# Kernel tuning notes

Hardware: AMD Instinct MI355X
Metric: run time of the kernel (lower is better)

## Reference

```python
import jax, jax.numpy as jnp
import numpy as np

B, Q, KV = 4, 256, 1024
QS, KS, H, VS = 128, 128, 128, 256

def setup_inputs() -> dict:
    key = jax.random.key(0)
    ks = jax.random.split(key, 7)
    return {
        "queries": jax.random.normal(ks[0], (B, Q, QS), dtype=jnp.float32),
        "keys": jax.random.normal(ks[1], (B, KV, KS), dtype=jnp.float32),
        "values": jax.random.normal(ks[2], (B, KV, VS), dtype=jnp.float32),
        "valid_lens": jax.random.randint(ks[3], (B,), 0, KV, dtype=jnp.int64 if jax.config.read('jax_enable_x64') else jnp.int32),
        "Wq": jax.random.normal(ks[4], (QS, H), dtype=jnp.float32),
        "Wk": jax.random.normal(ks[5], (KS, H), dtype=jnp.float32),
        "wv": jax.random.normal(ks[6], (H,), dtype=jnp.float32),
    }

def reference(queries, keys, values, valid_lens, Wq, Wk, wv):
    # project: [B,Q,H], [B,KV,H]
    q = jnp.einsum('bqd,dh->bqh', queries, Wq)
    k = jnp.einsum('bkd,dh->bkh', keys, Wk)
    # additive scores: broadcast add -> tanh -> reduce with w_v  [B,Q,KV]
    feats = jnp.tanh(q[:, :, None, :] + k[:, None, :, :])  # [B,Q,KV,H]
    scores = jnp.einsum('bqkh,h->bqk', feats, wv)
    # masked softmax over KV with value -1e6 at masked slots
    mask = jnp.arange(scores.shape[-1])[None, None, :] < valid_lens[:, None, None]
    scores = jnp.where(mask, scores, -1e6)
    attn = jax.nn.softmax(scores, axis=-1)
    # weighted sum of values  [B,Q,VS]
    return jnp.einsum('bqk,bkv->bqv', attn, values)
```

## Files before the change

kernel.cpp:

```cpp
#include <hip/hip_runtime.h>

#define LOG2E   1.4426950408889634f

__global__ __launch_bounds__(256) void proj_kernel(
    const float* __restrict__ q_in, const float* __restrict__ k_in,
    const float* __restrict__ Wq, const float* __restrict__ Wk,
    const int* __restrict__ valid_lens,
    float* __restrict__ qc, float* __restrict__ kct)
{
    __shared__ __align__(16) float x_s[8][128];
    __shared__ __align__(16) float ps[4][8][128];
    int tid = threadIdx.x;
    int blk = blockIdx.x;
    bool is_q = (blk < 128);
    int r0 = (is_q ? blk : blk - 128) * 8;
    int bb = r0 >> 10;
    if (!is_q) {
        int vl = valid_lens[bb];
        if ((r0 & 1023) >= vl) return;
    }
    const float* X = (is_q ? q_in : k_in) + (size_t)r0 * 128;
    const float* W = is_q ? Wq : Wk;

    *(float4*)&x_s[tid >> 5][(tid & 31) * 4] = ((const float4*)X)[tid];
    __syncthreads();

    int hl = tid & 63;
    int dq = tid >> 6;
    float a0[8] = {0,0,0,0,0,0,0,0};
    float a1[8] = {0,0,0,0,0,0,0,0};
#pragma unroll
    for (int i4 = 0; i4 < 8; ++i4) {
        int d = dq*32 + i4*4;
        float w00 = W[(d+0)*128 + hl], w01 = W[(d+0)*128 + hl + 64];
        float w10 = W[(d+1)*128 + hl], w11 = W[(d+1)*128 + hl + 64];
        float w20 = W[(d+2)*128 + hl], w21 = W[(d+2)*128 + hl + 64];
        float w30 = W[(d+3)*128 + hl], w31 = W[(d+3)*128 + hl + 64];
#pragma unroll
        for (int r = 0; r < 8; ++r) {
            float4 xv = *(const float4*)&x_s[r][d];
            a0[r] = fmaf(xv.x,w00, fmaf(xv.y,w10, fmaf(xv.z,w20, fmaf(xv.w,w30, a0[r]))));
            a1[r] = fmaf(xv.x,w01, fmaf(xv.y,w11, fmaf(xv.z,w21, fmaf(xv.w,w31, a1[r]))));
        }
    }
#pragma unroll
    for (int r = 0; r < 8; ++r) {
        ps[dq][r][hl]      = a0[r];
        ps[dq][r][hl + 64] = a1[r];
    }
    __syncthreads();

    int r  = tid >> 5;
    int c4 = (tid & 31) * 4;
    float4 s0 = *(const float4*)&ps[0][r][c4];
    float4 s1 = *(const float4*)&ps[1][r][c4];
    float4 s2 = *(const float4*)&ps[2][r][c4];
    float4 s3 = *(const float4*)&ps[3][r][c4];
    float4 v;
    v.x = __builtin_amdgcn_exp2f(((s0.x+s1.x)+(s2.x+s3.x))*LOG2E);
    v.y = __builtin_amdgcn_exp2f(((s0.y+s1.y)+(s2.y+s3.y))*LOG2E);
    v.z = __builtin_amdgcn_exp2f(((s0.z+s1.z)+(s2.z+s3.z))*LOG2E);
    v.w = __builtin_amdgcn_exp2f(((s0.w+s1.w)+(s2.w+s3.w))*LOG2E);
    if (is_q) {
        *(float4*)&qc[(size_t)(r0 + r)*128 + c4] = v;
    } else {
        int c    = (r0 & 1023) >> 6;
        int kvin = (r0 & 63) + r;
        *(float4*)&kct[((((size_t)(bb*16 + c))*32 + (c4 >> 2))*64 + kvin)*4] = v;
    }
}

__global__ __launch_bounds__(512, 8) void attn_split_kernel(
    const float* __restrict__ qc, const float* __restrict__ kct,
    const float* __restrict__ values, const int* __restrict__ valid_lens,
    const float* __restrict__ wv, float* __restrict__ pO, float* __restrict__ pml)
{
    __shared__ float2 e2_s[512];
    __shared__ float4 po[8][2][64];
    __shared__ float2 red_m[8], red_s[8];

    int tid  = threadIdx.x;
    int b    = blockIdx.y;
    int q0   = blockIdx.x * 2;
    int s    = blockIdx.z;
    int w    = tid >> 6;
    int lane = tid & 63;
    int vl   = valid_lens[b];
    int row0 = b*256 + q0;

    if (s == 1 && vl > 0 && vl <= 512) {
        if (tid < 2) pml[(size_t)(1024 + row0 + tid)*2] = -1e30f;
        return;
    }

    const float4* qa4 = (const float4*)(qc + (size_t)row0*128);
    const float4* qb4 = qa4 + 32;
    const float4* wv4 = (const float4*)wv;
    const float4* p0  = (const float4*)kct + ((size_t)(b*16 + s*8 + w))*2048 + lane;

    float a00 = 0.f, a10 = 0.f;
    if ((s*8 + w)*64 < vl) {
#pragma unroll 4
        for (int hb = 0; hb < 32; ++hb) {
            float4 wvv = wv4[hb];
            float4 qa = qa4[hb], qb = qb4[hb];
            float4 k0 = p0[(size_t)hb*64];
            float t;
            t = qa.x*k0.x; a00 = fmaf(wvv.x, __builtin_amdgcn_rcpf(fmaf(t,t,1.f)), a00);
            t = qb.x*k0.x; a10 = fmaf(wvv.x, __builtin_amdgcn_rcpf(fmaf(t,t,1.f)), a10);
            t = qa.y*k0.y; a00 = fmaf(wvv.y, __builtin_amdgcn_rcpf(fmaf(t,t,1.f)), a00);
            t = qb.y*k0.y; a10 = fmaf(wvv.y, __builtin_amdgcn_rcpf(fmaf(t,t,1.f)), a10);
            t = qa.z*k0.z; a00 = fmaf(wvv.z, __builtin_amdgcn_rcpf(fmaf(t,t,1.f)), a00);
            t = qb.z*k0.z; a10 = fmaf(wvv.z, __builtin_amdgcn_rcpf(fmaf(t,t,1.f)), a10);
            t = qa.w*k0.w; a00 = fmaf(wvv.w, __builtin_amdgcn_rcpf(fmaf(t,t,1.f)), a00);
            t = qb.w*k0.w; a10 = fmaf(wvv.w, __builtin_amdgcn_rcpf(fmaf(t,t,1.f)), a10);
        }
    }

    int lkv = w*64 + lane;
    bool valid = (s*512 + lkv < vl);
    float s00 = valid ? -2.f*a00 : -1e6f;
    float s10 = valid ? -2.f*a10 : -1e6f;

    float m0 = s00, m1 = s10;
#pragma unroll
    for (int off = 32; off; off >>= 1) {
        m0 = fmaxf(m0, __shfl_xor(m0, off));
        m1 = fmaxf(m1, __shfl_xor(m1, off));
    }
    if (lane == 0) red_m[w] = make_float2(m0, m1);
    __syncthreads();
    {
        float2 mm = red_m[0];
#pragma unroll
        for (int ww = 1; ww < 8; ++ww) {
            float2 t = red_m[ww];
            mm.x = fmaxf(mm.x, t.x); mm.y = fmaxf(mm.y, t.y);
        }
        m0 = mm.x; m1 = mm.y;
    }

    float e00 = __builtin_amdgcn_exp2f((s00 - m0) * LOG2E);
    float e10 = __builtin_amdgcn_exp2f((s10 - m1) * LOG2E);
    e2_s[lkv] = make_float2(e00, e10);
    float l0 = e00, l1 = e10;
#pragma unroll
    for (int off = 32; off; off >>= 1) {
        l0 += __shfl_xor(l0, off);
        l1 += __shfl_xor(l1, off);
    }
    if (lane == 0) red_s[w] = make_float2(l0, l1);
    __syncthreads();

    int local_end = (vl == 0) ? 512 : min(512, vl - s*512);
    float4 ac0 = {0,0,0,0}, ac1 = {0,0,0,0};
    const float4* V4 = (const float4*)values + (size_t)b*65536 + (size_t)s*512*64 + lane;
#pragma unroll 2
    for (int k2 = w; k2 < local_end; k2 += 8) {
        float4 vv = V4[(size_t)k2*64];
        float2 ee = e2_s[k2];
        ac0.x = fmaf(ee.x, vv.x, ac0.x); ac0.y = fmaf(ee.x, vv.y, ac0.y);
        ac0.z = fmaf(ee.x, vv.z, ac0.z); ac0.w = fmaf(ee.x, vv.w, ac0.w);
        ac1.x = fmaf(ee.y, vv.x, ac1.x); ac1.y = fmaf(ee.y, vv.y, ac1.y);
        ac1.z = fmaf(ee.y, vv.z, ac1.z); ac1.w = fmaf(ee.y, vv.w, ac1.w);
    }
    po[w][0][lane] = ac0;
    po[w][1][lane] = ac1;

    if (tid < 2) {
        float lsum = 0.f;
#pragma unroll
        for (int ww = 0; ww < 8; ++ww) {
            float2 t = red_s[ww];
            lsum += tid ? t.y : t.x;
        }
        float mm = tid ? m1 : m0;
        *(float2*)&pml[(size_t)(s*1024 + row0 + tid)*2] = make_float2(mm, lsum);
    }
    __syncthreads();

    int qq  = tid >> 8;
    int col = tid & 255;
    const float* pp = (const float*)po;
    float r = 0.f;
#pragma unroll
    for (int ww = 0; ww < 8; ++ww) r += pp[(ww*2 + qq)*256 + col];
    pO[(size_t)(s*1024 + row0 + qq)*256 + col] = r;
}

__global__ __launch_bounds__(256) void combine_kernel(
    const float* __restrict__ pO, const float* __restrict__ pml,
    float* __restrict__ out)
{
    int tid  = threadIdx.x;
    int row  = blockIdx.x*4 + (tid >> 6);
    int lane = tid & 63;
    float2 ml0 = *(const float2*)&pml[(size_t)row*2];
    float2 ml1 = *(const float2*)&pml[(size_t)(1024 + row)*2];
    float m  = fmaxf(ml0.x, ml1.x);
    float w0 = __builtin_amdgcn_exp2f((ml0.x - m) * LOG2E);
    float w1 = __builtin_amdgcn_exp2f((ml1.x - m) * LOG2E);
    float inv = 1.0f / (w0*ml0.y + w1*ml1.y);
    float4 o0 = ((const float4*)pO)[(size_t)row*64 + lane];
    float4 o1 = ((const float4*)pO)[(size_t)(1024 + row)*64 + lane];
    float4 o;
    o.x = (w0*o0.x + w1*o1.x) * inv;
    o.y = (w0*o0.y + w1*o1.y) * inv;
    o.z = (w0*o0.z + w1*o1.z) * inv;
    o.w = (w0*o0.w + w1*o1.w) * inv;
    ((float4*)out)[(size_t)row*64 + lane] = o;
}

extern "C" void kernel_launch(void* const* d_in, const int* in_sizes, int n_in,
                              void* d_out, int out_size, void* d_ws, size_t ws_size,
                              hipStream_t stream)
{
    const float* queries = (const float*)d_in[0];
    const float* keys    = (const float*)d_in[1];
    const float* values  = (const float*)d_in[2];
    const int*   vlens   = (const int*)d_in[3];
    const float* Wq      = (const float*)d_in[4];
    const float* Wk      = (const float*)d_in[5];
    const float* wv      = (const float*)d_in[6];
    float* out = (float*)d_out;

    float* qc  = (float*)d_ws;
    float* kct = qc  + 4*256*128;
    float* pO  = kct + 4*16*32*64*4;
    float* pml = pO  + 2*1024*256;

    proj_kernel<<<640, 256, 0, stream>>>(queries, keys, Wq, Wk, vlens, qc, kct);
    attn_split_kernel<<<dim3(128, 4, 2), 512, 0, stream>>>(qc, kct, values, vlens, wv, pO, pml);
    combine_kernel<<<256, 256, 0, stream>>>(pO, pml, out);
}
```

Before: 92.61 us.

## Pre-convert values to packed fp16 pairs and use fdot2 in the P·V loop

Adds extra blocks to the projection kernel that convert the fp32 values tensor into fp16, packing two consecutive KV rows per 32-bit word. The attention kernel then reads this half-size buffer and accumulates with v_dot2 fp16 dot products, converting the softmax weights to fp16 on the fly. The aim is to halve the value-read traffic and instruction count in the weighted-sum loop. In exchange it adds a full conversion pass over all values, independent of valid_lens, and loses precision from round-toward-zero fp16 weights and values.

```diff
diff --git a/kernel.cpp b/kernel.cpp
--- a/kernel.cpp
+++ b/kernel.cpp
@@ -1,17 +1,44 @@
 #include <hip/hip_runtime.h>
 
 #define LOG2E   1.4426950408889634f
+
+typedef _Float16 fh2 __attribute__((ext_vector_type(2)));
+typedef __fp16   ph2 __attribute__((ext_vector_type(2)));
+union h2u { fh2 f; ph2 p; unsigned int u; };
+__device__ __forceinline__ unsigned int pk2bits(ph2 h) { h2u t; t.p = h; return t.u; }
+__device__ __forceinline__ fh2 pk2f(ph2 h) { h2u t; t.p = h; return t.f; }
+__device__ __forceinline__ fh2 bits2f(unsigned int u) { h2u t; t.u = u; return t.f; }
 
 __global__ __launch_bounds__(256) void proj_kernel(
     const float* __restrict__ q_in, const float* __restrict__ k_in,
+    const float* __restrict__ v_in,
     const float* __restrict__ Wq, const float* __restrict__ Wk,
     const int* __restrict__ valid_lens,
-    float* __restrict__ qc, float* __restrict__ kct)
+    float* __restrict__ qc, float* __restrict__ kct,
+    unsigned int* __restrict__ vh)
 {
     __shared__ __align__(16) float x_s[8][128];
     __shared__ __align__(16) float ps[4][8][128];
     int tid = threadIdx.x;
     int blk = blockIdx.x;
+
+    if (blk >= 640) {
+        int vb = blk - 640;
+        int P  = vb*4 + (tid >> 6);
+        int bb = P >> 9, p = P & 511;
+        int lane = tid & 63;
+        const float4* r0 = (const float4*)(v_in + ((size_t)(bb*1024 + 2*p))*256) + lane;
+        float4 x0 = r0[0];
+        float4 x1 = r0[64];
+        uint4 h;
+        h.x = pk2bits(__builtin_amdgcn_cvt_pkrtz(x0.x, x1.x));
+        h.y = pk2bits(__builtin_amdgcn_cvt_pkrtz(x0.y, x1.y));
+        h.z = pk2bits(__builtin_amdgcn_cvt_pkrtz(x0.z, x1.z));
+        h.w = pk2bits(__builtin_amdgcn_cvt_pkrtz(x0.w, x1.w));
+        ((uint4*)vh)[(size_t)P*64 + lane] = h;
+        return;
+    }
+
     bool is_q = (blk < 128);
     int r0 = (is_q ? blk : blk - 128) * 8;
     int bb = r0 >> 10;
@@ -72,10 +99,10 @@
 
 __global__ __launch_bounds__(512, 8) void attn_split_kernel(
     const float* __restrict__ qc, const float* __restrict__ kct,
-    const float* __restrict__ values, const int* __restrict__ valid_lens,
+    const unsigned int* __restrict__ vh, const int* __restrict__ valid_lens,
     const float* __restrict__ wv, float* __restrict__ pO, float* __restrict__ pml)
 {
-    __shared__ float2 e2_s[512];
+    __shared__ __align__(16) float2 e2_s[512];
     __shared__ float4 po[8][2][64];
     __shared__ float2 red_m[8], red_s[8];
 
@@ -153,16 +180,25 @@
     __syncthreads();
 
     int local_end = (vl == 0) ? 512 : min(512, vl - s*512);
+    int pair_end  = (local_end + 1) >> 1;
     float4 ac0 = {0,0,0,0}, ac1 = {0,0,0,0};
-    const float4* V4 = (const float4*)values + (size_t)b*65536 + (size_t)s*512*64 + lane;
+    const uint4* VH = (const uint4*)vh + ((size_t)b*512 + (size_t)s*256)*64 + lane;
 #pragma unroll 2
-    for (int k2 = w; k2 < local_end; k2 += 8) {
-        float4 vv = V4[(size_t)k2*64];
-        float2 ee = e2_s[k2];
-        ac0.x = fmaf(ee.x, vv.x, ac0.x); ac0.y = fmaf(ee.x, vv.y, ac0.y);
-        ac0.z = fmaf(ee.x, vv.z, ac0.z); ac0.w = fmaf(ee.x, vv.w, ac0.w);
-        ac1.x = fmaf(ee.y, vv.x, ac1.x); ac1.y = fmaf(ee.y, vv.y, ac1.y);
-        ac1.z = fmaf(ee.y, vv.z, ac1.z); ac1.w = fmaf(ee.y, vv.w, ac1.w);
+    for (int p = w; p < pair_end; p += 8) {
+        uint4 vv = VH[(size_t)p*64];
+        float4 E = *(const float4*)&e2_s[2*p];
+        fh2 eh0 = pk2f(__builtin_amdgcn_cvt_pkrtz(E.x, E.z));
+        fh2 eh1 = pk2f(__builtin_amdgcn_cvt_pkrtz(E.y, E.w));
+        fh2 v0 = bits2f(vv.x), v1 = bits2f(vv.y);
+        fh2 v2 = bits2f(vv.z), v3 = bits2f(vv.w);
+        ac0.x = __builtin_amdgcn_fdot2(eh0, v0, ac0.x, false);
+        ac0.y = __builtin_amdgcn_fdot2(eh0, v1, ac0.y, false);
+        ac0.z = __builtin_amdgcn_fdot2(eh0, v2, ac0.z, false);
+        ac0.w = __builtin_amdgcn_fdot2(eh0, v3, ac0.w, false);
+        ac1.x = __builtin_amdgcn_fdot2(eh1, v0, ac1.x, false);
+        ac1.y = __builtin_amdgcn_fdot2(eh1, v1, ac1.y, false);
+        ac1.z = __builtin_amdgcn_fdot2(eh1, v2, ac1.z, false);
+        ac1.w = __builtin_amdgcn_fdot2(eh1, v3, ac1.w, false);
     }
     po[w][0][lane] = ac0;
     po[w][1][lane] = ac1;
@@ -228,8 +264,9 @@
     float* kct = qc  + 4*256*128;
     float* pO  = kct + 4*16*32*64*4;
     float* pml = pO  + 2*1024*256;
-
-    proj_kernel<<<640, 256, 0, stream>>>(queries, keys, Wq, Wk, vlens, qc, kct);
-    attn_split_kernel<<<dim3(128, 4, 2), 512, 0, stream>>>(qc, kct, values, vlens, wv, pO, pml);
+    unsigned int* vh = (unsigned int*)(pml + 2*1024*2);
+
+    proj_kernel<<<1152, 256, 0, stream>>>(queries, keys, values, Wq, Wk, vlens, qc, kct, vh);
+    attn_split_kernel<<<dim3(128, 4, 2), 512, 0, stream>>>(qc, kct, vh, vlens, wv, pO, pml);
     combine_kernel<<<256, 256, 0, stream>>>(pO, pml, out);
 }
```

After: 88.68 us. -4.2%, faster.
